# Performance work log

Hardware: AMD Instinct MI355X
Metric: run time of the kernel (lower is better)

The kernel has to match this reference:

```python
import jax, jax.numpy as jnp
import numpy as np

K = 512
D = 64
N = 262144


def setup_inputs() -> dict:
    key = jax.random.key(0)
    k1, k2 = jax.random.split(key)
    z_e_x = jax.random.normal(k1, (N, D), dtype=jnp.float32)
    # nn.Embedding(K, D) with uniform_(-1/K, 1/K)
    codebook = jax.random.uniform(k2, (K, D), dtype=jnp.float32,
                                  minval=-1.0 / K, maxval=1.0 / K)
    return {"z_e_x": z_e_x, "codebook": codebook}


def _vq_indices(x_flat, codebook):
    c_sqr = jnp.sum(codebook * codebook, axis=1)          # [K]
    x_sqr = jnp.sum(x_flat * x_flat, axis=1, keepdims=True)  # [N,1]
    distances = x_sqr + c_sqr - 2.0 * (x_flat @ codebook.T)  # [N,K]
    return jnp.argmin(distances, axis=1)                  # [N] int


def reference(z_e_x, codebook):
    # VQEmbedding.straight_through with inactive_count=None
    x_flat = z_e_x.reshape(-1, codebook.shape[1])
    indices = _vq_indices(x_flat, codebook)
    # z_q_x: lookup into detached codebook
    z_q_x = codebook[indices].reshape(z_e_x.shape)
    # z_q_x_bar: lookup into live codebook (same values in fwd)
    z_q_x_bar = codebook[indices].reshape(z_e_x.shape)
    return z_q_x, z_q_x_bar, indices
```

## Files before the change

kernel.cpp:

```cpp
#include <hip/hip_runtime.h>
#include <math.h>

#define KCODES 512
#define DDIM   64
#define NROWS  262144
#define ND     ((size_t)NROWS * DDIM)
#define MBLK   64
#define MARGIN 1.5e-4f


typedef __attribute__((ext_vector_type(8))) short s16x8;
typedef __attribute__((ext_vector_type(4))) float f32x4;
union U4S8 { uint4 u; s16x8 s; };

__device__ __forceinline__ unsigned short bf16_rne(float f) {
    unsigned u = __float_as_uint(f);
    return (unsigned short)((u + 0x7FFFu + ((u >> 16) & 1u)) >> 16);
}
__device__ __forceinline__ float bf16_tof(unsigned short h) {
    return __uint_as_float(((unsigned)h) << 16);
}

__device__ __forceinline__ void g2lds16(const void* g, void* l) {
    __builtin_amdgcn_global_load_lds(
        (const __attribute__((address_space(1))) unsigned int*)g,
        (__attribute__((address_space(3))) unsigned int*)l,
        16, 0, 0);
}

__device__ __forceinline__ float np_sumsq64(const float* v) {
    float r[8];
#pragma unroll
    for (int j = 0; j < 8; ++j) r[j] = __fmul_rn(v[j], v[j]);
#pragma unroll
    for (int i = 8; i < 64; i += 8) {
#pragma unroll
        for (int j = 0; j < 8; ++j)
            r[j] = __fadd_rn(r[j], __fmul_rn(v[i + j], v[i + j]));
    }
    float t01 = __fadd_rn(r[0], r[1]);
    float t23 = __fadd_rn(r[2], r[3]);
    float t45 = __fadd_rn(r[4], r[5]);
    float t67 = __fadd_rn(r[6], r[7]);
    return __fadd_rn(__fadd_rn(t01, t23), __fadd_rn(t45, t67));
}

__device__ __forceinline__ float np_xs_stream(const float4* __restrict__ xr) {
    float4 u = xr[0], w = xr[1];
    float r0 = __fmul_rn(u.x, u.x), r1 = __fmul_rn(u.y, u.y);
    float r2 = __fmul_rn(u.z, u.z), r3 = __fmul_rn(u.w, u.w);
    float r4 = __fmul_rn(w.x, w.x), r5 = __fmul_rn(w.y, w.y);
    float r6 = __fmul_rn(w.z, w.z), r7 = __fmul_rn(w.w, w.w);
#pragma unroll
    for (int i = 1; i < 8; ++i) {
        u = xr[2 * i]; w = xr[2 * i + 1];
        r0 = __fadd_rn(r0, __fmul_rn(u.x, u.x));
        r1 = __fadd_rn(r1, __fmul_rn(u.y, u.y));
        r2 = __fadd_rn(r2, __fmul_rn(u.z, u.z));
        r3 = __fadd_rn(r3, __fmul_rn(u.w, u.w));
        r4 = __fadd_rn(r4, __fmul_rn(w.x, w.x));
        r5 = __fadd_rn(r5, __fmul_rn(w.y, w.y));
        r6 = __fadd_rn(r6, __fmul_rn(w.z, w.z));
        r7 = __fadd_rn(r7, __fmul_rn(w.w, w.w));
    }
    float t01 = __fadd_rn(r0, r1), t23 = __fadd_rn(r2, r3);
    float t45 = __fadd_rn(r4, r5), t67 = __fadd_rn(r6, r7);
    return __fadd_rn(__fadd_rn(t01, t23), __fadd_rn(t45, t67));
}

__device__ __forceinline__ float dot_seq(const float4* __restrict__ xr,
                                         const float* __restrict__ c) {
    const float4* c4 = (const float4*)c;
    float a = 0.f;
#pragma unroll
    for (int i = 0; i < 16; ++i) {
        float4 xv = xr[i];
        float4 cv = c4[i];
        a = __fmaf_rn(xv.x, cv.x, a);
        a = __fmaf_rn(xv.y, cv.y, a);
        a = __fmaf_rn(xv.z, cv.z, a);
        a = __fmaf_rn(xv.w, cv.w, a);
    }
    return a;
}

__global__ void vq_prep(const float* __restrict__ cb, float* __restrict__ cs,
                        unsigned short* __restrict__ FR) {
    int k = blockIdx.x * blockDim.x + threadIdx.x;
    if (k < KCODES) {
        float v[DDIM];
        const float4* c4 = (const float4*)(cb + (size_t)k * DDIM);
#pragma unroll
        for (int i = 0; i < DDIM / 4; ++i) {
            float4 t = c4[i];
            v[4 * i + 0] = t.x; v[4 * i + 1] = t.y;
            v[4 * i + 2] = t.z; v[4 * i + 3] = t.w;
        }
        cs[k] = np_sumsq64(v);
        int p = k >> 7, tt = (k >> 4) & 7, mm = k & 15;
        size_t rec = ((size_t)p * 8 + (size_t)tt) * 4;
#pragma unroll
        for (int d = 0; d < DDIM; ++d) {
            unsigned short h = bf16_rne(v[d]);
            unsigned short l = bf16_rne(v[d] - bf16_tof(h));
            int quad = (d >> 3) & 3;
            int j = d & 7;
            int fhi = d >> 5;
            int lane = quad * 16 + mm;
            FR[((rec + fhi) * 64 + lane) * 8 + j] = h;
            FR[((rec + 2 + fhi) * 64 + lane) * 8 + j] = l;
        }
    }
}

__device__ __forceinline__ void pack8(float4 a, float4 b, uint4& hi, uint4& lo) {
    unsigned short h0 = bf16_rne(a.x), h1 = bf16_rne(a.y),
                   h2 = bf16_rne(a.z), h3 = bf16_rne(a.w);
    unsigned short h4 = bf16_rne(b.x), h5 = bf16_rne(b.y),
                   h6 = bf16_rne(b.z), h7 = bf16_rne(b.w);
    unsigned short l0 = bf16_rne(a.x - bf16_tof(h0)), l1 = bf16_rne(a.y - bf16_tof(h1)),
                   l2 = bf16_rne(a.z - bf16_tof(h2)), l3 = bf16_rne(a.w - bf16_tof(h3));
    unsigned short l4 = bf16_rne(b.x - bf16_tof(h4)), l5 = bf16_rne(b.y - bf16_tof(h5)),
                   l6 = bf16_rne(b.z - bf16_tof(h6)), l7 = bf16_rne(b.w - bf16_tof(h7));
    hi.x = (unsigned)h0 | ((unsigned)h1 << 16); hi.y = (unsigned)h2 | ((unsigned)h3 << 16);
    hi.z = (unsigned)h4 | ((unsigned)h5 << 16); hi.w = (unsigned)h6 | ((unsigned)h7 << 16);
    lo.x = (unsigned)l0 | ((unsigned)l1 << 16); lo.y = (unsigned)l2 | ((unsigned)l3 << 16);
    lo.z = (unsigned)l4 | ((unsigned)l5 << 16); lo.w = (unsigned)l6 | ((unsigned)l7 << 16);
}

#define SMEM_BYTES 37376

__launch_bounds__(256, 4)
__global__ void vq_main(const float* __restrict__ x, const float* __restrict__ cb,
                        const float* __restrict__ cs,
                        const unsigned short* __restrict__ FR,
                        float* __restrict__ out) {
    extern __shared__ char smem[];
    uint4* SB   = (uint4*)(smem);
    int*   cnt  = (int*)  (smem + 32768);
    int*   lstk = (int*)  (smem + 33024);
    float* lsts = (float*)(smem + 35072);
    int*   win  = (int*)  (smem + 37120);

    const int t    = threadIdx.x;
    const int ln   = t & 63;
    const int wv   = t >> 6;
    const int m    = ln & 15;
    const int quad = ln >> 4;
    const int rowBlk0 = blockIdx.x * MBLK;

    {
        const char* gsrc = (const char*)FR;
#pragma unroll
        for (int i = 0; i < 8; ++i)
            g2lds16(gsrc + (size_t)(i * 256 + wv * 64 + ln) * 16,
                    (char*)SB + (size_t)(i * 256 + wv * 64) * 16);
    }

    if (t < 64) cnt[t] = 0;

    const float* xrow = x + (size_t)(rowBlk0 + wv * 16 + m) * DDIM + quad * 8;
    U4S8 axh0, axh1, axl0, axl1;
    {
        float4 a0 = *(const float4*)(xrow);
        float4 b0 = *(const float4*)(xrow + 4);
        float4 a1 = *(const float4*)(xrow + 32);
        float4 b1 = *(const float4*)(xrow + 36);
        pack8(a0, b0, axh0.u, axl0.u);
        pack8(a1, b1, axh1.u, axl1.u);
    }

    float rm[4] = {INFINITY, INFINITY, INFINITY, INFINITY};

    for (int p = 0; p < 4; ++p) {
        __syncthreads();

        float csr[8];
#pragma unroll
        for (int tt = 0; tt < 8; ++tt) csr[tt] = cs[p * 128 + tt * 16 + m];

        float s[4][8];
#pragma unroll
        for (int tt = 0; tt < 8; ++tt) {
            U4S8 bh0, bh1, bl0, bl1;
            bh0.u = SB[(tt * 4 + 0) * 64 + ln];
            bh1.u = SB[(tt * 4 + 1) * 64 + ln];
            bl0.u = SB[(tt * 4 + 2) * 64 + ln];
            bl1.u = SB[(tt * 4 + 3) * 64 + ln];
            f32x4 acc = {0.f, 0.f, 0.f, 0.f};
            acc = __builtin_amdgcn_mfma_f32_16x16x32_bf16(axh0.s, bh0.s, acc, 0, 0, 0);
            acc = __builtin_amdgcn_mfma_f32_16x16x32_bf16(axh1.s, bh1.s, acc, 0, 0, 0);
            acc = __builtin_amdgcn_mfma_f32_16x16x32_bf16(axl0.s, bh0.s, acc, 0, 0, 0);
            acc = __builtin_amdgcn_mfma_f32_16x16x32_bf16(axl1.s, bh1.s, acc, 0, 0, 0);
            acc = __builtin_amdgcn_mfma_f32_16x16x32_bf16(axh0.s, bl0.s, acc, 0, 0, 0);
            acc = __builtin_amdgcn_mfma_f32_16x16x32_bf16(axh1.s, bl1.s, acc, 0, 0, 0);
#pragma unroll
            for (int r = 0; r < 4; ++r)
                s[r][tt] = __fmaf_rn(-2.0f, acc[r], csr[tt]);
        }

        __syncthreads();

        if (p < 3) {
            const char* gsrc = (const char*)FR + (size_t)(p + 1) * 32768;
#pragma unroll
            for (int i = 0; i < 8; ++i)
                g2lds16(gsrc + (size_t)(i * 256 + wv * 64 + ln) * 16,
                        (char*)SB + (size_t)(i * 256 + wv * 64) * 16);
        }

#pragma unroll
        for (int r = 0; r < 4; ++r) {
            float mn = s[r][0];
#pragma unroll
            for (int tt = 1; tt < 8; ++tt) mn = fminf(mn, s[r][tt]);
            mn = fminf(mn, __shfl_xor(mn, 1, 64));
            mn = fminf(mn, __shfl_xor(mn, 2, 64));
            mn = fminf(mn, __shfl_xor(mn, 4, 64));
            mn = fminf(mn, __shfl_xor(mn, 8, 64));
            rm[r] = fminf(rm[r], mn);
        }
#pragma unroll
        for (int r = 0; r < 4; ++r) {
            float thr = rm[r] + MARGIN;
            int lrow = wv * 16 + quad * 4 + r;
#pragma unroll
            for (int tt = 0; tt < 8; ++tt) {
                if (s[r][tt] <= thr) {
                    int pos = atomicAdd(&cnt[lrow], 1);
                    if (pos < 8) {
                        lstk[lrow * 8 + pos] = p * 128 + tt * 16 + m;
                        lsts[lrow * 8 + pos] = s[r][tt];
                    }
                }
            }
        }
    }

    __syncthreads();

    if (m < 4) {
        int lrow = wv * 16 + quad * 4 + m;
        float rmf = (m == 0) ? rm[0] : (m == 1) ? rm[1] : (m == 2) ? rm[2] : rm[3];
        float thr = rmf + MARGIN;
        int c = cnt[lrow];
        int kb;
        const float4* xr = (const float4*)(x + (size_t)(rowBlk0 + lrow) * DDIM);
        if (c <= 8) {
            int nc = 0, cand[8];
            for (int i = 0; i < c; ++i)
                if (lsts[lrow * 8 + i] <= thr) cand[nc++] = lstk[lrow * 8 + i];
            if (nc == 1) {
                kb = cand[0];
            } else {
                float xs = np_xs_stream(xr);
                float db = INFINITY; kb = 0x7fffffff;
                for (int j = 0; j < nc; ++j) {
                    int k = cand[j];
                    float a = dot_seq(xr, cb + (size_t)k * DDIM);
                    float d = __fadd_rn(__fadd_rn(xs, cs[k]), __fmul_rn(-2.0f, a));
                    if (d < db || (d == db && k < kb)) { db = d; kb = k; }
                }
            }
        } else {
            float xs = np_xs_stream(xr);
            float db = INFINITY; kb = 0;
            for (int k = 0; k < KCODES; ++k) {
                float a = dot_seq(xr, cb + (size_t)k * DDIM);
                float d = __fadd_rn(__fadd_rn(xs, cs[k]), __fmul_rn(-2.0f, a));
                if (d < db) { db = d; kb = k; }
            }
        }
        win[lrow] = kb;
        out[2 * ND + (size_t)(rowBlk0 + lrow)] = (float)kb;
    }
    __syncthreads();

#pragma unroll
    for (int i = 0; i < 4; ++i) {
        int g   = t + i * 256;
        int row = g >> 4, cc = g & 15;
        int kb  = win[row];
        float4 v = *(const float4*)(cb + (size_t)kb * DDIM + cc * 4);
        size_t gr = (size_t)(rowBlk0 + row) * DDIM + (size_t)cc * 4;
        *(float4*)(out + gr) = v;
        *(float4*)(out + ND + gr) = v;
    }
}

extern "C" void kernel_launch(void* const* d_in, const int* in_sizes, int n_in,
                              void* d_out, int out_size, void* d_ws, size_t ws_size,
                              hipStream_t stream) {
    const float* z  = (const float*)d_in[0];
    const float* cb = (const float*)d_in[1];
    float* out = (float*)d_out;
    float* cs          = (float*)d_ws;
    unsigned short* FR = (unsigned short*)((char*)d_ws + 2048);

    (void)hipFuncSetAttribute((const void*)vq_main,
                              hipFuncAttributeMaxDynamicSharedMemorySize,
                              SMEM_BYTES);
    vq_prep<<<2, 256, 0, stream>>>(cb, cs, FR);
    vq_main<<<NROWS / MBLK, 256, SMEM_BYTES, stream>>>(z, cb, cs, FR, out);
}
```

Before: 243.5 us.

## Process two row tiles per block, fold codebook norms into MFMA accumulators

Doubles rows per block so each wave reuses the same LDS codebook fragments for two 16-row tiles, halving LDS traffic and codebook staging per row. Seeds MFMA accumulators with -0.5*||c||^2 and switches to max-based selection, which removes the per-element FMA epilogue. Splits each chunk into halves so candidate filtering of the first half interleaves with MFMAs of the second. Also uses v_cvt_pk_bf16_f32 for packing, parallelises the prep kernel over more blocks, and shrinks the candidate cap to 6. The cost is higher register pressure under the same launch bounds, and a smaller cap sends more rows to the full 512-code fallback.

```diff
diff --git a/kernel.cpp b/kernel.cpp
--- a/kernel.cpp
+++ b/kernel.cpp
@@ -5,8 +5,9 @@
 #define DDIM   64
 #define NROWS  262144
 #define ND     ((size_t)NROWS * DDIM)
-#define MBLK   64
-#define MARGIN 1.5e-4f
+#define MBLK   128
+#define CAP    6
+#define MARGIN_HALF 7.5e-5f
 
 
 typedef __attribute__((ext_vector_type(8))) short s16x8;
@@ -19,6 +20,11 @@
 }
 __device__ __forceinline__ float bf16_tof(unsigned short h) {
     return __uint_as_float(((unsigned)h) << 16);
+}
+__device__ __forceinline__ unsigned cvtpk_bf16(float a, float b) {
+    unsigned r;
+    asm("v_cvt_pk_bf16_f32 %0, %1, %2" : "=v"(r) : "v"(a), "v"(b));
+    return r;
 }
 
 __device__ __forceinline__ void g2lds16(const void* g, void* l) {
@@ -84,63 +90,86 @@
     return a;
 }
 
+__device__ __forceinline__ unsigned pair_pack(float va, float vb, int lo) {
+    unsigned short ha = bf16_rne(va), hb = bf16_rne(vb);
+    if (lo) {
+        ha = bf16_rne(va - bf16_tof(ha));
+        hb = bf16_rne(vb - bf16_tof(hb));
+    }
+    return (unsigned)ha | ((unsigned)hb << 16);
+}
+
 __global__ void vq_prep(const float* __restrict__ cb, float* __restrict__ cs,
-                        unsigned short* __restrict__ FR) {
-    int k = blockIdx.x * blockDim.x + threadIdx.x;
-    if (k < KCODES) {
-        float v[DDIM];
-        const float4* c4 = (const float4*)(cb + (size_t)k * DDIM);
-#pragma unroll
-        for (int i = 0; i < DDIM / 4; ++i) {
-            float4 t = c4[i];
-            v[4 * i + 0] = t.x; v[4 * i + 1] = t.y;
-            v[4 * i + 2] = t.z; v[4 * i + 3] = t.w;
-        }
-        cs[k] = np_sumsq64(v);
-        int p = k >> 7, tt = (k >> 4) & 7, mm = k & 15;
-        size_t rec = ((size_t)p * 8 + (size_t)tt) * 4;
-#pragma unroll
-        for (int d = 0; d < DDIM; ++d) {
-            unsigned short h = bf16_rne(v[d]);
-            unsigned short l = bf16_rne(v[d] - bf16_tof(h));
-            int quad = (d >> 3) & 3;
-            int j = d & 7;
-            int fhi = d >> 5;
-            int lane = quad * 16 + mm;
-            FR[((rec + fhi) * 64 + lane) * 8 + j] = h;
-            FR[((rec + 2 + fhi) * 64 + lane) * 8 + j] = l;
+                        float* __restrict__ csh, unsigned short* __restrict__ FR) {
+    int bid = blockIdx.x, t = threadIdx.x;
+    if (bid < 32) {
+        int g = bid * 256 + t;
+        int lane = g & 63, fr = (g >> 6) & 3, tt = (g >> 8) & 7, p = g >> 11;
+        int mm = lane & 15, quad = lane >> 4;
+        int k = p * 128 + tt * 16 + mm;
+        int d0 = (fr & 1) * 32 + quad * 8;
+        int lo = fr >> 1;
+        const float* src = cb + (size_t)k * DDIM + d0;
+        float4 a = *(const float4*)src;
+        float4 b = *(const float4*)(src + 4);
+        uint4 pk;
+        pk.x = pair_pack(a.x, a.y, lo);
+        pk.y = pair_pack(a.z, a.w, lo);
+        pk.z = pair_pack(b.x, b.y, lo);
+        pk.w = pair_pack(b.z, b.w, lo);
+        ((uint4*)FR)[g] = pk;
+    } else {
+        int k = (bid - 32) * 256 + t;
+        if (k < KCODES) {
+            float v[DDIM];
+            const float4* c4 = (const float4*)(cb + (size_t)k * DDIM);
+#pragma unroll
+            for (int i = 0; i < DDIM / 4; ++i) {
+                float4 tv = c4[i];
+                v[4 * i + 0] = tv.x; v[4 * i + 1] = tv.y;
+                v[4 * i + 2] = tv.z; v[4 * i + 3] = tv.w;
+            }
+            float s = np_sumsq64(v);
+            cs[k] = s;
+            csh[k] = -0.5f * s;
         }
     }
 }
 
 __device__ __forceinline__ void pack8(float4 a, float4 b, uint4& hi, uint4& lo) {
-    unsigned short h0 = bf16_rne(a.x), h1 = bf16_rne(a.y),
-                   h2 = bf16_rne(a.z), h3 = bf16_rne(a.w);
-    unsigned short h4 = bf16_rne(b.x), h5 = bf16_rne(b.y),
-                   h6 = bf16_rne(b.z), h7 = bf16_rne(b.w);
-    unsigned short l0 = bf16_rne(a.x - bf16_tof(h0)), l1 = bf16_rne(a.y - bf16_tof(h1)),
-                   l2 = bf16_rne(a.z - bf16_tof(h2)), l3 = bf16_rne(a.w - bf16_tof(h3));
-    unsigned short l4 = bf16_rne(b.x - bf16_tof(h4)), l5 = bf16_rne(b.y - bf16_tof(h5)),
-                   l6 = bf16_rne(b.z - bf16_tof(h6)), l7 = bf16_rne(b.w - bf16_tof(h7));
-    hi.x = (unsigned)h0 | ((unsigned)h1 << 16); hi.y = (unsigned)h2 | ((unsigned)h3 << 16);
-    hi.z = (unsigned)h4 | ((unsigned)h5 << 16); hi.w = (unsigned)h6 | ((unsigned)h7 << 16);
-    lo.x = (unsigned)l0 | ((unsigned)l1 << 16); lo.y = (unsigned)l2 | ((unsigned)l3 << 16);
-    lo.z = (unsigned)l4 | ((unsigned)l5 << 16); lo.w = (unsigned)l6 | ((unsigned)l7 << 16);
-}
-
-#define SMEM_BYTES 37376
+    hi.x = cvtpk_bf16(a.x, a.y);
+    hi.y = cvtpk_bf16(a.z, a.w);
+    hi.z = cvtpk_bf16(b.x, b.y);
+    hi.w = cvtpk_bf16(b.z, b.w);
+    float r0 = a.x - __uint_as_float(hi.x << 16);
+    float r1 = a.y - __uint_as_float(hi.x & 0xffff0000u);
+    float r2 = a.z - __uint_as_float(hi.y << 16);
+    float r3 = a.w - __uint_as_float(hi.y & 0xffff0000u);
+    float r4 = b.x - __uint_as_float(hi.z << 16);
+    float r5 = b.y - __uint_as_float(hi.z & 0xffff0000u);
+    float r6 = b.z - __uint_as_float(hi.w << 16);
+    float r7 = b.w - __uint_as_float(hi.w & 0xffff0000u);
+    lo.x = cvtpk_bf16(r0, r1);
+    lo.y = cvtpk_bf16(r2, r3);
+    lo.z = cvtpk_bf16(r4, r5);
+    lo.w = cvtpk_bf16(r6, r7);
+}
+
+#define SMEM_BYTES 39936
+
+#define MFMA16(A, B, C) __builtin_amdgcn_mfma_f32_16x16x32_bf16((A).s, (B).s, (C), 0, 0, 0)
 
 __launch_bounds__(256, 4)
 __global__ void vq_main(const float* __restrict__ x, const float* __restrict__ cb,
-                        const float* __restrict__ cs,
+                        const float* __restrict__ cs, const float* __restrict__ csh,
                         const unsigned short* __restrict__ FR,
                         float* __restrict__ out) {
     extern __shared__ char smem[];
     uint4* SB   = (uint4*)(smem);
     int*   cnt  = (int*)  (smem + 32768);
-    int*   lstk = (int*)  (smem + 33024);
-    float* lsts = (float*)(smem + 35072);
-    int*   win  = (int*)  (smem + 37120);
+    int*   lstk = (int*)  (smem + 33280);
+    float* lsts = (float*)(smem + 36352);
+    int*   win  = (int*)  (smem + 39424);
 
     const int t    = threadIdx.x;
     const int ln   = t & 63;
@@ -156,47 +185,117 @@
             g2lds16(gsrc + (size_t)(i * 256 + wv * 64 + ln) * 16,
                     (char*)SB + (size_t)(i * 256 + wv * 64) * 16);
     }
-
-    if (t < 64) cnt[t] = 0;
-
-    const float* xrow = x + (size_t)(rowBlk0 + wv * 16 + m) * DDIM + quad * 8;
-    U4S8 axh0, axh1, axl0, axl1;
+    if (t < 128) cnt[t] = 0;
+
+    const float* xrow0 = x + (size_t)(rowBlk0 + wv * 16 + m) * DDIM + quad * 8;
+    const float* xrow1 = xrow0 + (size_t)64 * DDIM;
+    U4S8 ah0A, ah1A, al0A, al1A, ah0B, ah1B, al0B, al1B;
     {
-        float4 a0 = *(const float4*)(xrow);
-        float4 b0 = *(const float4*)(xrow + 4);
-        float4 a1 = *(const float4*)(xrow + 32);
-        float4 b1 = *(const float4*)(xrow + 36);
-        pack8(a0, b0, axh0.u, axl0.u);
-        pack8(a1, b1, axh1.u, axl1.u);
-    }
-
-    float rm[4] = {INFINITY, INFINITY, INFINITY, INFINITY};
+        float4 a0 = *(const float4*)(xrow0);
+        float4 b0 = *(const float4*)(xrow0 + 4);
+        float4 a1 = *(const float4*)(xrow0 + 32);
+        float4 b1 = *(const float4*)(xrow0 + 36);
+        pack8(a0, b0, ah0A.u, al0A.u);
+        pack8(a1, b1, ah1A.u, al1A.u);
+        a0 = *(const float4*)(xrow1);      b0 = *(const float4*)(xrow1 + 4);
+        a1 = *(const float4*)(xrow1 + 32); b1 = *(const float4*)(xrow1 + 36);
+        pack8(a0, b0, ah0B.u, al0B.u);
+        pack8(a1, b1, ah1B.u, al1B.u);
+    }
+
+    float rm0[4] = {-INFINITY, -INFINITY, -INFINITY, -INFINITY};
+    float rm1[4] = {-INFINITY, -INFINITY, -INFINITY, -INFINITY};
 
     for (int p = 0; p < 4; ++p) {
         __syncthreads();
 
-        float csr[8];
-#pragma unroll
-        for (int tt = 0; tt < 8; ++tt) csr[tt] = cs[p * 128 + tt * 16 + m];
-
-        float s[4][8];
-#pragma unroll
-        for (int tt = 0; tt < 8; ++tt) {
+        float chv[8];
+#pragma unroll
+        for (int tt = 0; tt < 8; ++tt) chv[tt] = csh[p * 128 + tt * 16 + m];
+
+        f32x4 sA[4], sB[4];
+
+#pragma unroll
+        for (int q = 0; q < 4; ++q) {
+            const int tt = q;
             U4S8 bh0, bh1, bl0, bl1;
             bh0.u = SB[(tt * 4 + 0) * 64 + ln];
             bh1.u = SB[(tt * 4 + 1) * 64 + ln];
             bl0.u = SB[(tt * 4 + 2) * 64 + ln];
             bl1.u = SB[(tt * 4 + 3) * 64 + ln];
-            f32x4 acc = {0.f, 0.f, 0.f, 0.f};
-            acc = __builtin_amdgcn_mfma_f32_16x16x32_bf16(axh0.s, bh0.s, acc, 0, 0, 0);
-            acc = __builtin_amdgcn_mfma_f32_16x16x32_bf16(axh1.s, bh1.s, acc, 0, 0, 0);
-            acc = __builtin_amdgcn_mfma_f32_16x16x32_bf16(axl0.s, bh0.s, acc, 0, 0, 0);
-            acc = __builtin_amdgcn_mfma_f32_16x16x32_bf16(axl1.s, bh1.s, acc, 0, 0, 0);
-            acc = __builtin_amdgcn_mfma_f32_16x16x32_bf16(axh0.s, bl0.s, acc, 0, 0, 0);
-            acc = __builtin_amdgcn_mfma_f32_16x16x32_bf16(axh1.s, bl1.s, acc, 0, 0, 0);
-#pragma unroll
-            for (int r = 0; r < 4; ++r)
-                s[r][tt] = __fmaf_rn(-2.0f, acc[r], csr[tt]);
+            float ch = chv[tt];
+            f32x4 a0 = {ch, ch, ch, ch}, a1 = {ch, ch, ch, ch};
+            __builtin_amdgcn_s_setprio(1);
+            a0 = MFMA16(ah0A, bh0, a0); a1 = MFMA16(ah0B, bh0, a1);
+            a0 = MFMA16(ah1A, bh1, a0); a1 = MFMA16(ah1B, bh1, a1);
+            a0 = MFMA16(al0A, bh0, a0); a1 = MFMA16(al0B, bh0, a1);
+            a0 = MFMA16(al1A, bh1, a0); a1 = MFMA16(al1B, bh1, a1);
+            a0 = MFMA16(ah0A, bl0, a0); a1 = MFMA16(ah0B, bl0, a1);
+            a0 = MFMA16(ah1A, bl1, a0); a1 = MFMA16(ah1B, bl1, a1);
+            __builtin_amdgcn_s_setprio(0);
+            sA[q] = a0; sB[q] = a1;
+        }
+        {
+            const int kbase = p * 128;
+#pragma unroll
+            for (int r = 0; r < 4; ++r) {
+                float mx = fmaxf(fmaxf(sA[0][r], sA[1][r]), fmaxf(sA[2][r], sA[3][r]));
+                mx = fmaxf(mx, __shfl_xor(mx, 1));
+                mx = fmaxf(mx, __shfl_xor(mx, 2));
+                mx = fmaxf(mx, __shfl_xor(mx, 4));
+                mx = fmaxf(mx, __shfl_xor(mx, 8));
+                rm0[r] = fmaxf(rm0[r], mx);
+                float my = fmaxf(fmaxf(sB[0][r], sB[1][r]), fmaxf(sB[2][r], sB[3][r]));
+                my = fmaxf(my, __shfl_xor(my, 1));
+                my = fmaxf(my, __shfl_xor(my, 2));
+                my = fmaxf(my, __shfl_xor(my, 4));
+                my = fmaxf(my, __shfl_xor(my, 8));
+                rm1[r] = fmaxf(rm1[r], my);
+            }
+#pragma unroll
+            for (int r = 0; r < 4; ++r) {
+                int lrow0 = wv * 16 + quad * 4 + r;
+                float th0 = rm0[r] - MARGIN_HALF;
+                float th1 = rm1[r] - MARGIN_HALF;
+#pragma unroll
+                for (int q = 0; q < 4; ++q) {
+                    if (sA[q][r] >= th0) {
+                        int pos = atomicAdd(&cnt[lrow0], 1);
+                        if (pos < CAP) {
+                            lstk[lrow0 * CAP + pos] = kbase + q * 16 + m;
+                            lsts[lrow0 * CAP + pos] = sA[q][r];
+                        }
+                    }
+                    if (sB[q][r] >= th1) {
+                        int pos = atomicAdd(&cnt[lrow0 + 64], 1);
+                        if (pos < CAP) {
+                            lstk[(lrow0 + 64) * CAP + pos] = kbase + q * 16 + m;
+                            lsts[(lrow0 + 64) * CAP + pos] = sB[q][r];
+                        }
+                    }
+                }
+            }
+        }
+
+#pragma unroll
+        for (int q = 0; q < 4; ++q) {
+            const int tt = 4 + q;
+            U4S8 bh0, bh1, bl0, bl1;
+            bh0.u = SB[(tt * 4 + 0) * 64 + ln];
+            bh1.u = SB[(tt * 4 + 1) * 64 + ln];
+            bl0.u = SB[(tt * 4 + 2) * 64 + ln];
+            bl1.u = SB[(tt * 4 + 3) * 64 + ln];
+            float ch = chv[tt];
+            f32x4 a0 = {ch, ch, ch, ch}, a1 = {ch, ch, ch, ch};
+            __builtin_amdgcn_s_setprio(1);
+            a0 = MFMA16(ah0A, bh0, a0); a1 = MFMA16(ah0B, bh0, a1);
+            a0 = MFMA16(ah1A, bh1, a0); a1 = MFMA16(ah1B, bh1, a1);
+            a0 = MFMA16(al0A, bh0, a0); a1 = MFMA16(al0B, bh0, a1);
+            a0 = MFMA16(al1A, bh1, a0); a1 = MFMA16(al1B, bh1, a1);
+            a0 = MFMA16(ah0A, bl0, a0); a1 = MFMA16(ah0B, bl0, a1);
+            a0 = MFMA16(ah1A, bl1, a0); a1 = MFMA16(ah1B, bl1, a1);
+            __builtin_amdgcn_s_setprio(0);
+            sA[q] = a0; sB[q] = a1;
         }
 
         __syncthreads();
@@ -209,28 +308,43 @@
                         (char*)SB + (size_t)(i * 256 + wv * 64) * 16);
         }
 
-#pragma unroll
-        for (int r = 0; r < 4; ++r) {
-            float mn = s[r][0];
-#pragma unroll
-            for (int tt = 1; tt < 8; ++tt) mn = fminf(mn, s[r][tt]);
-            mn = fminf(mn, __shfl_xor(mn, 1, 64));
-            mn = fminf(mn, __shfl_xor(mn, 2, 64));
-            mn = fminf(mn, __shfl_xor(mn, 4, 64));
-            mn = fminf(mn, __shfl_xor(mn, 8, 64));
-            rm[r] = fminf(rm[r], mn);
-        }
-#pragma unroll
-        for (int r = 0; r < 4; ++r) {
-            float thr = rm[r] + MARGIN;
-            int lrow = wv * 16 + quad * 4 + r;
-#pragma unroll
-            for (int tt = 0; tt < 8; ++tt) {
-                if (s[r][tt] <= thr) {
-                    int pos = atomicAdd(&cnt[lrow], 1);
-                    if (pos < 8) {
-                        lstk[lrow * 8 + pos] = p * 128 + tt * 16 + m;
-                        lsts[lrow * 8 + pos] = s[r][tt];
+        {
+            const int kbase = p * 128 + 64;
+#pragma unroll
+            for (int r = 0; r < 4; ++r) {
+                float mx = fmaxf(fmaxf(sA[0][r], sA[1][r]), fmaxf(sA[2][r], sA[3][r]));
+                mx = fmaxf(mx, __shfl_xor(mx, 1));
+                mx = fmaxf(mx, __shfl_xor(mx, 2));
+                mx = fmaxf(mx, __shfl_xor(mx, 4));
+                mx = fmaxf(mx, __shfl_xor(mx, 8));
+                rm0[r] = fmaxf(rm0[r], mx);
+                float my = fmaxf(fmaxf(sB[0][r], sB[1][r]), fmaxf(sB[2][r], sB[3][r]));
+                my = fmaxf(my, __shfl_xor(my, 1));
+                my = fmaxf(my, __shfl_xor(my, 2));
+                my = fmaxf(my, __shfl_xor(my, 4));
+                my = fmaxf(my, __shfl_xor(my, 8));
+                rm1[r] = fmaxf(rm1[r], my);
+            }
+#pragma unroll
+            for (int r = 0; r < 4; ++r) {
+                int lrow0 = wv * 16 + quad * 4 + r;
+                float th0 = rm0[r] - MARGIN_HALF;
+                float th1 = rm1[r] - MARGIN_HALF;
+#pragma unroll
+                for (int q = 0; q < 4; ++q) {
+                    if (sA[q][r] >= th0) {
+                        int pos = atomicAdd(&cnt[lrow0], 1);
+                        if (pos < CAP) {
+                            lstk[lrow0 * CAP + pos] = kbase + q * 16 + m;
+                            lsts[lrow0 * CAP + pos] = sA[q][r];
+                        }
+                    }
+                    if (sB[q][r] >= th1) {
+                        int pos = atomicAdd(&cnt[lrow0 + 64], 1);
+                        if (pos < CAP) {
+                            lstk[(lrow0 + 64) * CAP + pos] = kbase + q * 16 + m;
+                            lsts[(lrow0 + 64) * CAP + pos] = sB[q][r];
+                        }
                     }
                 }
             }
@@ -239,27 +353,35 @@
 
     __syncthreads();
 
-    if (m < 4) {
-        int lrow = wv * 16 + quad * 4 + m;
-        float rmf = (m == 0) ? rm[0] : (m == 1) ? rm[1] : (m == 2) ? rm[2] : rm[3];
-        float thr = rmf + MARGIN;
+    if (m < 8) {
+        int r = m & 3;
+        int set1 = m >> 2;
+        int lrow = set1 * 64 + wv * 16 + quad * 4 + r;
+        float v0 = set1 ? rm1[0] : rm0[0];
+        float v1 = set1 ? rm1[1] : rm0[1];
+        float v2 = set1 ? rm1[2] : rm0[2];
+        float v3 = set1 ? rm1[3] : rm0[3];
+        float rmf = (r == 0) ? v0 : (r == 1) ? v1 : (r == 2) ? v2 : v3;
+        float thr = rmf - MARGIN_HALF;
         int c = cnt[lrow];
         int kb;
         const float4* xr = (const float4*)(x + (size_t)(rowBlk0 + lrow) * DDIM);
-        if (c <= 8) {
-            int nc = 0, cand[8];
+        if (c <= CAP) {
+            int nc = 0, k1 = 0;
             for (int i = 0; i < c; ++i)
-                if (lsts[lrow * 8 + i] <= thr) cand[nc++] = lstk[lrow * 8 + i];
+                if (lsts[lrow * CAP + i] >= thr) { ++nc; k1 = lstk[lrow * CAP + i]; }
             if (nc == 1) {
-                kb = cand[0];
+                kb = k1;
             } else {
                 float xs = np_xs_stream(xr);
                 float db = INFINITY; kb = 0x7fffffff;
-                for (int j = 0; j < nc; ++j) {
-                    int k = cand[j];
-                    float a = dot_seq(xr, cb + (size_t)k * DDIM);
-                    float d = __fadd_rn(__fadd_rn(xs, cs[k]), __fmul_rn(-2.0f, a));
-                    if (d < db || (d == db && k < kb)) { db = d; kb = k; }
+                for (int i = 0; i < c; ++i) {
+                    if (lsts[lrow * CAP + i] >= thr) {
+                        int k = lstk[lrow * CAP + i];
+                        float a = dot_seq(xr, cb + (size_t)k * DDIM);
+                        float d = __fadd_rn(__fadd_rn(xs, cs[k]), __fmul_rn(-2.0f, a));
+                        if (d < db || (d == db && k < kb)) { db = d; kb = k; }
+                    }
                 }
             }
         } else {
@@ -277,7 +399,7 @@
     __syncthreads();
 
 #pragma unroll
-    for (int i = 0; i < 4; ++i) {
+    for (int i = 0; i < 8; ++i) {
         int g   = t + i * 256;
         int row = g >> 4, cc = g & 15;
         int kb  = win[row];
@@ -295,11 +417,12 @@
     const float* cb = (const float*)d_in[1];
     float* out = (float*)d_out;
     float* cs          = (float*)d_ws;
-    unsigned short* FR = (unsigned short*)((char*)d_ws + 2048);
+    float* csh         = (float*)((char*)d_ws + 2048);
+    unsigned short* FR = (unsigned short*)((char*)d_ws + 4096);
 
     (void)hipFuncSetAttribute((const void*)vq_main,
                               hipFuncAttributeMaxDynamicSharedMemorySize,
                               SMEM_BYTES);
-    vq_prep<<<2, 256, 0, stream>>>(cb, cs, FR);
-    vq_main<<<NROWS / MBLK, 256, SMEM_BYTES, stream>>>(z, cb, cs, FR, out);
-}
+    vq_prep<<<34, 256, 0, stream>>>(cb, cs, csh, FR);
+    vq_main<<<NROWS / MBLK, 256, SMEM_BYTES, stream>>>(z, cb, cs, csh, FR, out);
+}
```

Result: slower. 555.4 us (+128.1%).

## Fold -0.5*||c||^2 into MFMA accumulator init, parallelize codebook prep, use packed bf16 cvt

Applied to the files above, without the earlier changes.

The main loop now starts each MFMA accumulator at -0.5*||c||^2 and does an argmax of x·c - 0.5||c||^2, which drops the per-score FMA. The candidate margin is halved to match the rescaled scores. The prep kernel now spreads the bf16 hi/lo fragment packing over 32 blocks with coalesced uint4 writes, where before 512 threads did scattered 2-byte stores, and it also stores the halved negative norms. The activation split into bf16 hi/lo now uses the v_cvt_pk_bf16_f32 instruction, and the candidate array is replaced by a second pass over LDS.

```diff
diff --git a/kernel.cpp b/kernel.cpp
--- a/kernel.cpp
+++ b/kernel.cpp
@@ -6,7 +6,8 @@
 #define NROWS  262144
 #define ND     ((size_t)NROWS * DDIM)
 #define MBLK   64
-#define MARGIN 1.5e-4f
+#define CAP    8
+#define MARGIN_HALF 7.5e-5f
 
 
 typedef __attribute__((ext_vector_type(8))) short s16x8;
@@ -19,6 +20,11 @@
 }
 __device__ __forceinline__ float bf16_tof(unsigned short h) {
     return __uint_as_float(((unsigned)h) << 16);
+}
+__device__ __forceinline__ unsigned cvtpk_bf16(float a, float b) {
+    unsigned r;
+    asm("v_cvt_pk_bf16_f32 %0, %1, %2" : "=v"(r) : "v"(a), "v"(b));
+    return r;
 }
 
 __device__ __forceinline__ void g2lds16(const void* g, void* l) {
@@ -84,55 +90,76 @@
     return a;
 }
 
+__device__ __forceinline__ unsigned pair_pack(float va, float vb, int lo) {
+    unsigned short ha = bf16_rne(va), hb = bf16_rne(vb);
+    if (lo) {
+        ha = bf16_rne(va - bf16_tof(ha));
+        hb = bf16_rne(vb - bf16_tof(hb));
+    }
+    return (unsigned)ha | ((unsigned)hb << 16);
+}
+
 __global__ void vq_prep(const float* __restrict__ cb, float* __restrict__ cs,
-                        unsigned short* __restrict__ FR) {
-    int k = blockIdx.x * blockDim.x + threadIdx.x;
-    if (k < KCODES) {
-        float v[DDIM];
-        const float4* c4 = (const float4*)(cb + (size_t)k * DDIM);
-#pragma unroll
-        for (int i = 0; i < DDIM / 4; ++i) {
-            float4 t = c4[i];
-            v[4 * i + 0] = t.x; v[4 * i + 1] = t.y;
-            v[4 * i + 2] = t.z; v[4 * i + 3] = t.w;
-        }
-        cs[k] = np_sumsq64(v);
-        int p = k >> 7, tt = (k >> 4) & 7, mm = k & 15;
-        size_t rec = ((size_t)p * 8 + (size_t)tt) * 4;
-#pragma unroll
-        for (int d = 0; d < DDIM; ++d) {
-            unsigned short h = bf16_rne(v[d]);
-            unsigned short l = bf16_rne(v[d] - bf16_tof(h));
-            int quad = (d >> 3) & 3;
-            int j = d & 7;
-            int fhi = d >> 5;
-            int lane = quad * 16 + mm;
-            FR[((rec + fhi) * 64 + lane) * 8 + j] = h;
-            FR[((rec + 2 + fhi) * 64 + lane) * 8 + j] = l;
+                        float* __restrict__ csh, unsigned short* __restrict__ FR) {
+    int bid = blockIdx.x, t = threadIdx.x;
+    if (bid < 32) {
+        int g = bid * 256 + t;
+        int lane = g & 63, fr = (g >> 6) & 3, tt = (g >> 8) & 7, p = g >> 11;
+        int mm = lane & 15, quad = lane >> 4;
+        int k = p * 128 + tt * 16 + mm;
+        int d0 = (fr & 1) * 32 + quad * 8;
+        int lo = fr >> 1;
+        const float* src = cb + (size_t)k * DDIM + d0;
+        float4 a = *(const float4*)src;
+        float4 b = *(const float4*)(src + 4);
+        uint4 pk;
+        pk.x = pair_pack(a.x, a.y, lo);
+        pk.y = pair_pack(a.z, a.w, lo);
+        pk.z = pair_pack(b.x, b.y, lo);
+        pk.w = pair_pack(b.z, b.w, lo);
+        ((uint4*)FR)[g] = pk;
+    } else {
+        int k = (bid - 32) * 256 + t;
+        if (k < KCODES) {
+            float v[DDIM];
+            const float4* c4 = (const float4*)(cb + (size_t)k * DDIM);
+#pragma unroll
+            for (int i = 0; i < DDIM / 4; ++i) {
+                float4 tv = c4[i];
+                v[4 * i + 0] = tv.x; v[4 * i + 1] = tv.y;
+                v[4 * i + 2] = tv.z; v[4 * i + 3] = tv.w;
+            }
+            float s = np_sumsq64(v);
+            cs[k] = s;
+            csh[k] = -0.5f * s;
         }
     }
 }
 
 __device__ __forceinline__ void pack8(float4 a, float4 b, uint4& hi, uint4& lo) {
-    unsigned short h0 = bf16_rne(a.x), h1 = bf16_rne(a.y),
-                   h2 = bf16_rne(a.z), h3 = bf16_rne(a.w);
-    unsigned short h4 = bf16_rne(b.x), h5 = bf16_rne(b.y),
-                   h6 = bf16_rne(b.z), h7 = bf16_rne(b.w);
-    unsigned short l0 = bf16_rne(a.x - bf16_tof(h0)), l1 = bf16_rne(a.y - bf16_tof(h1)),
-                   l2 = bf16_rne(a.z - bf16_tof(h2)), l3 = bf16_rne(a.w - bf16_tof(h3));
-    unsigned short l4 = bf16_rne(b.x - bf16_tof(h4)), l5 = bf16_rne(b.y - bf16_tof(h5)),
-                   l6 = bf16_rne(b.z - bf16_tof(h6)), l7 = bf16_rne(b.w - bf16_tof(h7));
-    hi.x = (unsigned)h0 | ((unsigned)h1 << 16); hi.y = (unsigned)h2 | ((unsigned)h3 << 16);
-    hi.z = (unsigned)h4 | ((unsigned)h5 << 16); hi.w = (unsigned)h6 | ((unsigned)h7 << 16);
-    lo.x = (unsigned)l0 | ((unsigned)l1 << 16); lo.y = (unsigned)l2 | ((unsigned)l3 << 16);
-    lo.z = (unsigned)l4 | ((unsigned)l5 << 16); lo.w = (unsigned)l6 | ((unsigned)l7 << 16);
+    hi.x = cvtpk_bf16(a.x, a.y);
+    hi.y = cvtpk_bf16(a.z, a.w);
+    hi.z = cvtpk_bf16(b.x, b.y);
+    hi.w = cvtpk_bf16(b.z, b.w);
+    float r0 = a.x - __uint_as_float(hi.x << 16);
+    float r1 = a.y - __uint_as_float(hi.x & 0xffff0000u);
+    float r2 = a.z - __uint_as_float(hi.y << 16);
+    float r3 = a.w - __uint_as_float(hi.y & 0xffff0000u);
+    float r4 = b.x - __uint_as_float(hi.z << 16);
+    float r5 = b.y - __uint_as_float(hi.z & 0xffff0000u);
+    float r6 = b.z - __uint_as_float(hi.w << 16);
+    float r7 = b.w - __uint_as_float(hi.w & 0xffff0000u);
+    lo.x = cvtpk_bf16(r0, r1);
+    lo.y = cvtpk_bf16(r2, r3);
+    lo.z = cvtpk_bf16(r4, r5);
+    lo.w = cvtpk_bf16(r6, r7);
 }
 
 #define SMEM_BYTES 37376
 
 __launch_bounds__(256, 4)
 __global__ void vq_main(const float* __restrict__ x, const float* __restrict__ cb,
-                        const float* __restrict__ cs,
+                        const float* __restrict__ cs, const float* __restrict__ csh,
                         const unsigned short* __restrict__ FR,
                         float* __restrict__ out) {
     extern __shared__ char smem[];
@@ -170,14 +197,14 @@
         pack8(a1, b1, axh1.u, axl1.u);
     }
 
-    float rm[4] = {INFINITY, INFINITY, INFINITY, INFINITY};
+    float rm[4] = {-INFINITY, -INFINITY, -INFINITY, -INFINITY};
 
     for (int p = 0; p < 4; ++p) {
         __syncthreads();
 
-        float csr[8];
-#pragma unroll
-        for (int tt = 0; tt < 8; ++tt) csr[tt] = cs[p * 128 + tt * 16 + m];
+        float chv[8];
+#pragma unroll
+        for (int tt = 0; tt < 8; ++tt) chv[tt] = csh[p * 128 + tt * 16 + m];
 
         float s[4][8];
 #pragma unroll
@@ -187,7 +214,8 @@
             bh1.u = SB[(tt * 4 + 1) * 64 + ln];
             bl0.u = SB[(tt * 4 + 2) * 64 + ln];
             bl1.u = SB[(tt * 4 + 3) * 64 + ln];
-            f32x4 acc = {0.f, 0.f, 0.f, 0.f};
+            float ch = chv[tt];
+            f32x4 acc = {ch, ch, ch, ch};
             acc = __builtin_amdgcn_mfma_f32_16x16x32_bf16(axh0.s, bh0.s, acc, 0, 0, 0);
             acc = __builtin_amdgcn_mfma_f32_16x16x32_bf16(axh1.s, bh1.s, acc, 0, 0, 0);
             acc = __builtin_amdgcn_mfma_f32_16x16x32_bf16(axl0.s, bh0.s, acc, 0, 0, 0);
@@ -196,7 +224,7 @@
             acc = __builtin_amdgcn_mfma_f32_16x16x32_bf16(axh1.s, bl1.s, acc, 0, 0, 0);
 #pragma unroll
             for (int r = 0; r < 4; ++r)
-                s[r][tt] = __fmaf_rn(-2.0f, acc[r], csr[tt]);
+                s[r][tt] = acc[r];
         }
 
         __syncthreads();
@@ -211,26 +239,26 @@
 
 #pragma unroll
         for (int r = 0; r < 4; ++r) {
-            float mn = s[r][0];
-#pragma unroll
-            for (int tt = 1; tt < 8; ++tt) mn = fminf(mn, s[r][tt]);
-            mn = fminf(mn, __shfl_xor(mn, 1, 64));
-            mn = fminf(mn, __shfl_xor(mn, 2, 64));
-            mn = fminf(mn, __shfl_xor(mn, 4, 64));
-            mn = fminf(mn, __shfl_xor(mn, 8, 64));
-            rm[r] = fminf(rm[r], mn);
+            float mx = s[r][0];
+#pragma unroll
+            for (int tt = 1; tt < 8; ++tt) mx = fmaxf(mx, s[r][tt]);
+            mx = fmaxf(mx, __shfl_xor(mx, 1, 64));
+            mx = fmaxf(mx, __shfl_xor(mx, 2, 64));
+            mx = fmaxf(mx, __shfl_xor(mx, 4, 64));
+            mx = fmaxf(mx, __shfl_xor(mx, 8, 64));
+            rm[r] = fmaxf(rm[r], mx);
         }
 #pragma unroll
         for (int r = 0; r < 4; ++r) {
-            float thr = rm[r] + MARGIN;
+            float thr = rm[r] - MARGIN_HALF;
             int lrow = wv * 16 + quad * 4 + r;
 #pragma unroll
             for (int tt = 0; tt < 8; ++tt) {
-                if (s[r][tt] <= thr) {
+                if (s[r][tt] >= thr) {
                     int pos = atomicAdd(&cnt[lrow], 1);
-                    if (pos < 8) {
-                        lstk[lrow * 8 + pos] = p * 128 + tt * 16 + m;
-                        lsts[lrow * 8 + pos] = s[r][tt];
+                    if (pos < CAP) {
+                        lstk[lrow * CAP + pos] = p * 128 + tt * 16 + m;
+                        lsts[lrow * CAP + pos] = s[r][tt];
                     }
                 }
             }
@@ -242,24 +270,26 @@
     if (m < 4) {
         int lrow = wv * 16 + quad * 4 + m;
         float rmf = (m == 0) ? rm[0] : (m == 1) ? rm[1] : (m == 2) ? rm[2] : rm[3];
-        float thr = rmf + MARGIN;
+        float thr = rmf - MARGIN_HALF;
         int c = cnt[lrow];
         int kb;
         const float4* xr = (const float4*)(x + (size_t)(rowBlk0 + lrow) * DDIM);
-        if (c <= 8) {
-            int nc = 0, cand[8];
+        if (c <= CAP) {
+            int nc = 0, k1 = 0;
             for (int i = 0; i < c; ++i)
-                if (lsts[lrow * 8 + i] <= thr) cand[nc++] = lstk[lrow * 8 + i];
+                if (lsts[lrow * CAP + i] >= thr) { ++nc; k1 = lstk[lrow * CAP + i]; }
             if (nc == 1) {
-                kb = cand[0];
+                kb = k1;
             } else {
                 float xs = np_xs_stream(xr);
                 float db = INFINITY; kb = 0x7fffffff;
-                for (int j = 0; j < nc; ++j) {
-                    int k = cand[j];
-                    float a = dot_seq(xr, cb + (size_t)k * DDIM);
-                    float d = __fadd_rn(__fadd_rn(xs, cs[k]), __fmul_rn(-2.0f, a));
-                    if (d < db || (d == db && k < kb)) { db = d; kb = k; }
+                for (int i = 0; i < c; ++i) {
+                    if (lsts[lrow * CAP + i] >= thr) {
+                        int k = lstk[lrow * CAP + i];
+                        float a = dot_seq(xr, cb + (size_t)k * DDIM);
+                        float d = __fadd_rn(__fadd_rn(xs, cs[k]), __fmul_rn(-2.0f, a));
+                        if (d < db || (d == db && k < kb)) { db = d; kb = k; }
+                    }
                 }
             }
         } else {
@@ -295,11 +325,12 @@
     const float* cb = (const float*)d_in[1];
     float* out = (float*)d_out;
     float* cs          = (float*)d_ws;
-    unsigned short* FR = (unsigned short*)((char*)d_ws + 2048);
+    float* csh         = (float*)((char*)d_ws + 2048);
+    unsigned short* FR = (unsigned short*)((char*)d_ws + 4096);
 
     (void)hipFuncSetAttribute((const void*)vq_main,
                               hipFuncAttributeMaxDynamicSharedMemorySize,
                               SMEM_BYTES);
-    vq_prep<<<2, 256, 0, stream>>>(cb, cs, FR);
-    vq_main<<<NROWS / MBLK, 256, SMEM_BYTES, stream>>>(z, cb, cs, FR, out);
-}
+    vq_prep<<<34, 256, 0, stream>>>(cb, cs, csh, FR);
+    vq_main<<<NROWS / MBLK, 256, SMEM_BYTES, stream>>>(z, cb, cs, csh, FR, out);
+}
```

Result: faster. 236.4 us (-2.9%).
